# Optimization experiments

Hardware: AMD Instinct MI355X
Metric: run time of the kernel (lower is better)

The kernel has to match this reference:

```python
import jax, jax.numpy as jnp
import numpy as np

GRID_NUM = 7
IMG_SIZE = 448.0
LAMBDA_COORD = 5.0
LAMBDA_NOOBJ = 0.5
EPS = 1e-12
NUM_CLASSES = 20
BATCH = 16384


def setup_inputs() -> dict:
    key = jax.random.key(0)
    k1, k2, k3 = jax.random.split(key, 3)
    # predictions in [0,1) so sqrt(w+eps) is well-defined (as sigmoid outputs would be)
    y_pre = jax.random.uniform(k1, (BATCH, GRID_NUM, GRID_NUM, 30), dtype=jnp.float32)
    # ground truth: ch0 = class_id in {0..20} (0 => no object), ch1:5 = (cx,cy,w,h), rest bookkeeping
    cls = jax.random.randint(k2, (BATCH, GRID_NUM, GRID_NUM, 1), 0, NUM_CLASSES + 1).astype(jnp.float32)
    rest = jax.random.uniform(k3, (BATCH, GRID_NUM, GRID_NUM, 7), dtype=jnp.float32)
    y_true = jnp.concatenate([cls, rest], axis=-1)
    return {"y_pre": y_pre, "y_true": y_true}


def _iou(box_p, box_t):
    # boxes: [..., 4] = (cx, cy, w, h); cx,cy are offsets within the cell (scaled by
    # cell size), w,h are relative to the full image (scaled by img size).
    # The shared grid-cell offset added to both centers cancels in the IoU, so it is omitted.
    cell = IMG_SIZE / GRID_NUM
    cxp, cyp = box_p[..., 0] * cell, box_p[..., 1] * cell
    wp, hp = box_p[..., 2] * IMG_SIZE, box_p[..., 3] * IMG_SIZE
    cxt, cyt = box_t[..., 0] * cell, box_t[..., 1] * cell
    wt, ht = box_t[..., 2] * IMG_SIZE, box_t[..., 3] * IMG_SIZE
    iw = jnp.maximum(jnp.minimum(cxp + wp / 2, cxt + wt / 2) - jnp.maximum(cxp - wp / 2, cxt - wt / 2), 0.0)
    ih = jnp.maximum(jnp.minimum(cyp + hp / 2, cyt + ht / 2) - jnp.maximum(cyp - hp / 2, cyt - ht / 2), 0.0)
    inter = iw * ih
    union = wp * hp + wt * ht - inter
    return inter / (union + EPS)


def reference(y_pre, y_true):
    obj = (y_true[..., 0] != 0.0)                     # [B,S,S] bool
    tb = y_true[..., 1:5]                             # true box
    b1, b2 = y_pre[..., 0:4], y_pre[..., 5:9]          # two predicted boxes
    c1, c2 = y_pre[..., 4], y_pre[..., 9]              # predicted confidences

    iou1 = _iou(b1, tb)
    iou2 = _iou(b2, tb)

    def coord_loss(bp):
        xy = jnp.sum((bp[..., 0:2] - tb[..., 0:2]) ** 2, axis=-1)
        wh = jnp.sum((jnp.sqrt(bp[..., 2:4] + EPS) - jnp.sqrt(tb[..., 2:4] + EPS)) ** 2, axis=-1)
        return xy + wh

    cls_true = jax.nn.one_hot(y_true[..., 0].astype(jnp.int32) - 1, NUM_CLASSES, dtype=y_pre.dtype)
    cls_loss = jnp.sum((y_pre[..., 10:] - cls_true) ** 2, axis=-1)

    obj_loss = ((c1 - iou1) ** 2 + (c2 - iou2) ** 2
                + LAMBDA_COORD * (coord_loss(b1) + coord_loss(b2))
                + cls_loss)
    noobj_loss = LAMBDA_NOOBJ * (c1 ** 2 + c2 ** 2)

    loss = jnp.sum(jnp.where(obj, obj_loss, noobj_loss)) / y_pre.shape[0]
    return loss
```

## Files before the change

### kernel.cpp

```cpp
#include <hip/hip_runtime.h>

#define NCELLS (16384 * 7 * 7)
#define NBLK (NCELLS / 256)
#define NPART (NBLK * 4)
#define INV_BATCH (1.0f / 16384.0f)
#define EPS 1e-12f
#define IMG 448.0f
#define CELL (448.0f / 7.0f)
#define L_COORD 5.0f
#define L_NOOBJ 0.5f

__device__ __forceinline__ float iou_f(const float* bp, const float* bt) {
    float cxp = bp[0] * CELL, cyp = bp[1] * CELL;
    float wp  = bp[2] * IMG,  hp  = bp[3] * IMG;
    float cxt = bt[0] * CELL, cyt = bt[1] * CELL;
    float wt  = bt[2] * IMG,  ht  = bt[3] * IMG;
    float iw = fmaxf(fminf(cxp + wp * 0.5f, cxt + wt * 0.5f) -
                     fmaxf(cxp - wp * 0.5f, cxt - wt * 0.5f), 0.0f);
    float ih = fmaxf(fminf(cyp + hp * 0.5f, cyt + ht * 0.5f) -
                     fmaxf(cyp - hp * 0.5f, cyt - ht * 0.5f), 0.0f);
    float inter = iw * ih;
    float uni = wp * hp + wt * ht - inter;
    return inter / (uni + EPS);
}

__device__ __forceinline__ float coord_loss(const float* bp, const float* tb) {
    float xy = (bp[0] - tb[0]) * (bp[0] - tb[0]) + (bp[1] - tb[1]) * (bp[1] - tb[1]);
    float s2 = sqrtf(bp[2] + EPS) - sqrtf(tb[2] + EPS);
    float s3 = sqrtf(bp[3] + EPS) - sqrtf(tb[3] + EPS);
    return xy + s2 * s2 + s3 * s3;
}

__global__ void __launch_bounds__(256) yolo_partial_kernel(
        const float* __restrict__ y_pre,
        const float* __restrict__ y_true,
        float* __restrict__ partial) {
    __shared__ float4 sp4[1920];
    const int tid  = threadIdx.x;
    const int lane = tid & 63;
    const int w    = tid >> 6;

    const float4* g4 = reinterpret_cast<const float4*>(y_pre)
                     + (size_t)blockIdx.x * 1920 + w * 480;
    float4* l4 = sp4 + w * 480;

    {
        float4 a = g4[lane];
        float4 b = g4[lane + 64];
        float4 c = g4[lane + 128];
        float4 d = g4[lane + 192];
        l4[lane]       = a;
        l4[lane + 64]  = b;
        l4[lane + 128] = c;
        l4[lane + 192] = d;
    }
    {
        float4 a = g4[lane + 256];
        float4 b = g4[lane + 320];
        float4 c = g4[lane + 384];
        l4[lane + 256] = a;
        l4[lane + 320] = b;
        l4[lane + 384] = c;
        if (lane < 32) {
            float4 d = g4[lane + 448];
            l4[lane + 448] = d;
        }
    }

    const int cell = blockIdx.x * 256 + tid;
    float tv[8];
    {
        const float4* t4 = reinterpret_cast<const float4*>(y_true) + (size_t)cell * 2;
        float4 ta = t4[0], tb4 = t4[1];
        tv[0] = ta.x; tv[1] = ta.y; tv[2] = ta.z; tv[3] = ta.w;
        tv[4] = tb4.x; tv[5] = tb4.y; tv[6] = tb4.z; tv[7] = tb4.w;
    }

    float pv[30];
    {
        const float2* l2 = reinterpret_cast<const float2*>(
            reinterpret_cast<const float*>(sp4) + w * 1920 + lane * 30);
        #pragma unroll
        for (int i = 0; i < 15; ++i) {
            float2 v = l2[i];
            pv[2 * i]     = v.x;
            pv[2 * i + 1] = v.y;
        }
    }

    float c1 = pv[4], c2 = pv[9];
    float loss;
    if (tv[0] != 0.0f) {
        const float* tbx = tv + 1;
        float iou1 = iou_f(pv + 0, tbx);
        float iou2 = iou_f(pv + 5, tbx);
        float cl1 = coord_loss(pv + 0, tbx);
        float cl2 = coord_loss(pv + 5, tbx);
        int c = (int)tv[0] - 1;
        float cls = 0.0f;
        #pragma unroll
        for (int k = 0; k < 20; ++k) {
            float d = pv[10 + k] - (k == c ? 1.0f : 0.0f);
            cls += d * d;
        }
        float d1 = c1 - iou1, d2 = c2 - iou2;
        loss = d1 * d1 + d2 * d2 + L_COORD * (cl1 + cl2) + cls;
    } else {
        loss = L_NOOBJ * (c1 * c1 + c2 * c2);
    }
    float local = loss * INV_BATCH;

    #pragma unroll
    for (int off = 32; off > 0; off >>= 1)
        local += __shfl_down(local, off);

    if (lane == 0)
        partial[blockIdx.x * 4 + w] = local;
}

__global__ void __launch_bounds__(256) yolo_final_kernel(
        const float* __restrict__ partial,
        float* __restrict__ out) {
    const int tid = threadIdx.x;
    const float4* p4 = reinterpret_cast<const float4*>(partial);
    float local = 0.0f;
    #pragma unroll 4
    for (int i = tid; i < NPART / 4; i += 256) {
        float4 v = p4[i];
        local += (v.x + v.y) + (v.z + v.w);
    }
    #pragma unroll
    for (int off = 32; off > 0; off >>= 1)
        local += __shfl_down(local, off);

    __shared__ float wsum[4];
    if ((tid & 63) == 0) wsum[tid >> 6] = local;
    __syncthreads();
    if (tid == 0)
        out[0] = wsum[0] + wsum[1] + wsum[2] + wsum[3];
}

extern "C" void kernel_launch(void* const* d_in, const int* in_sizes, int n_in,
                              void* d_out, int out_size, void* d_ws, size_t ws_size,
                              hipStream_t stream) {
    const float* y_pre  = (const float*)d_in[0];
    const float* y_true = (const float*)d_in[1];
    float* out = (float*)d_out;
    float* partial = (float*)d_ws;

    yolo_partial_kernel<<<NBLK, 256, 0, stream>>>(y_pre, y_true, partial);
    yolo_final_kernel<<<1, 256, 0, stream>>>(partial, out);
}
```

Measured before the change: 27.22 us.

## Stage predictions via direct global-to-LDS loads and widen final reduction block

Replaces the register-staged copy of y_pre into shared memory with __builtin_amdgcn_global_load_lds, so the data goes straight from global memory into LDS without passing through VGPRs, followed by an explicit vmcnt wait. The final reduction kernel is also widened from 256 to 1024 threads to shorten its serial loop. The direct-to-LDS path relies on the per-lane 16-byte layout matching the old copy. No barrier is added, which is fine only because each wave reads only its own LDS region.

```diff
diff --git a/kernel.cpp b/kernel.cpp
--- a/kernel.cpp
+++ b/kernel.cpp
@@ -44,27 +44,18 @@
                      + (size_t)blockIdx.x * 1920 + w * 480;
     float4* l4 = sp4 + w * 480;
 
-    {
-        float4 a = g4[lane];
-        float4 b = g4[lane + 64];
-        float4 c = g4[lane + 128];
-        float4 d = g4[lane + 192];
-        l4[lane]       = a;
-        l4[lane + 64]  = b;
-        l4[lane + 128] = c;
-        l4[lane + 192] = d;
+    #pragma unroll
+    for (int b = 0; b < 7; ++b) {
+        __builtin_amdgcn_global_load_lds(
+            (const __attribute__((address_space(1))) void*)(g4 + b * 64 + lane),
+            (__attribute__((address_space(3))) void*)(l4 + b * 64),
+            16, 0, 0);
     }
-    {
-        float4 a = g4[lane + 256];
-        float4 b = g4[lane + 320];
-        float4 c = g4[lane + 384];
-        l4[lane + 256] = a;
-        l4[lane + 320] = b;
-        l4[lane + 384] = c;
-        if (lane < 32) {
-            float4 d = g4[lane + 448];
-            l4[lane + 448] = d;
-        }
+    if (lane < 32) {
+        __builtin_amdgcn_global_load_lds(
+            (const __attribute__((address_space(1))) void*)(g4 + 448 + lane),
+            (__attribute__((address_space(3))) void*)(l4 + 448),
+            16, 0, 0);
     }
 
     const int cell = blockIdx.x * 256 + tid;
@@ -75,6 +66,8 @@
         tv[0] = ta.x; tv[1] = ta.y; tv[2] = ta.z; tv[3] = ta.w;
         tv[4] = tb4.x; tv[5] = tb4.y; tv[6] = tb4.z; tv[7] = tb4.w;
     }
+
+    asm volatile("s_waitcnt vmcnt(0)" ::: "memory");
 
     float pv[30];
     {
@@ -118,14 +111,14 @@
         partial[blockIdx.x * 4 + w] = local;
 }
 
-__global__ void __launch_bounds__(256) yolo_final_kernel(
+__global__ void __launch_bounds__(1024) yolo_final_kernel(
         const float* __restrict__ partial,
         float* __restrict__ out) {
     const int tid = threadIdx.x;
     const float4* p4 = reinterpret_cast<const float4*>(partial);
     float local = 0.0f;
     #pragma unroll 4
-    for (int i = tid; i < NPART / 4; i += 256) {
+    for (int i = tid; i < NPART / 4; i += 1024) {
         float4 v = p4[i];
         local += (v.x + v.y) + (v.z + v.w);
     }
@@ -133,11 +126,15 @@
     for (int off = 32; off > 0; off >>= 1)
         local += __shfl_down(local, off);
 
-    __shared__ float wsum[4];
+    __shared__ float wsum[16];
     if ((tid & 63) == 0) wsum[tid >> 6] = local;
     __syncthreads();
-    if (tid == 0)
-        out[0] = wsum[0] + wsum[1] + wsum[2] + wsum[3];
+    if (tid == 0) {
+        float s = 0.0f;
+        #pragma unroll
+        for (int i = 0; i < 16; ++i) s += wsum[i];
+        out[0] = s;
+    }
 }
 
 extern "C" void kernel_launch(void* const* d_in, const int* in_sizes, int n_in,
@@ -149,5 +146,5 @@
     float* partial = (float*)d_ws;
 
     yolo_partial_kernel<<<NBLK, 256, 0, stream>>>(y_pre, y_true, partial);
-    yolo_final_kernel<<<1, 256, 0, stream>>>(partial, out);
+    yolo_final_kernel<<<1, 1024, 0, stream>>>(partial, out);
 }
```

New measurement: 25.89 us. -4.9%, faster.
